# Optimization experiments

Measured on AMD Instinct MI355X. Metric: run time of the kernel, lower is better.

Reference implementation:

```python
import jax, jax.numpy as jnp
import numpy as np

B, P, D, VP, VD = 256, 1152, 10, 8, 16
NUM_ITER = 3


def setup_inputs() -> dict:
    key = jax.random.key(0)
    k1, k2 = jax.random.split(key)
    x = jax.random.normal(k1, (B, P, VP, 1), dtype=jnp.float32)
    # learned transform matrices, init randn/100 as in the torch module
    W = jax.random.normal(k2, (P, D, VD, VP), dtype=jnp.float32) / 100.0
    return {"x": x, "W": W}


def _squash(s, axis):
    # v = ||s||^2/(1+||s||^2) * s/||s||
    sq = jnp.sum(s * s, axis=axis, keepdims=True)
    return s * sq / (1.0 + sq) / jnp.sqrt(sq + 1e-9)


def reference(x, W):
    xs = x[..., 0]                                      # [B,P,8]
    # u_hat[b,p,d,:] = W[p,d] @ x[b,p]  (no explicit stack/broadcast materialization)
    u_hat = jnp.einsum('pdij,bpj->bpdi', W, xs)          # [B,P,D,16]
    u_stop = jax.lax.stop_gradient(u_hat)
    b_ij = jnp.zeros((B, P, D, 1), dtype=u_hat.dtype)    # torch b_ij [B,P,D,1,1], trailing 1 dropped
    v = None
    for it in range(NUM_ITER):
        # faithful to source: softmax over torch dim=3 (size-1 axis) -> all ones
        c_ij = jax.nn.softmax(b_ij, axis=3)               # [B,P,D,1]
        u = u_hat if it == NUM_ITER - 1 else u_stop
        s_j = jnp.sum(c_ij * u, axis=1)                   # [B,D,16]
        v = _squash(s_j, axis=2)                          # [B,D,16]
        if it != NUM_ITER - 1:
            # agreement: u_hat^T v -> scalar per (b,p,d)
            upd = jnp.einsum('bpdi,bdi->bpd', u_hat, v)[..., None]
            b_ij = b_ij + upd
    return v[..., None]                                   # [B,D,16,1] matching torch output
```

## Files before the change

kernel.cpp:

```cpp
#include <hip/hip_runtime.h>
#include <hip/hip_bf16.h>
#include <math.h>

#define M 256
#define N 160
#define K 9216
#define CH 72
#define KC 128
#define BM 32
#define WPS 1296
#define XSTR 136

using f32x4 = __attribute__((ext_vector_type(4))) float;
using bf16x8 = __attribute__((ext_vector_type(8))) short;

__device__ __forceinline__ ushort f2bf(float f) {
  return __builtin_bit_cast(ushort, __float2bfloat16(f));
}

template <bool ATOMIC>
__global__ __launch_bounds__(256) void gemm_mfma(const float* __restrict__ x,
                                                 const float* __restrict__ W,
                                                 float* __restrict__ part) {
  __shared__ __align__(16) ushort Wl[2][4 * WPS];
  __shared__ __align__(16) ushort Xl[BM * XSTR];

  const int t = threadIdx.x;
  const int bx = blockIdx.x;
  const int mt = bx & 7;
  const int c = bx >> 3;
  const int m0 = mt * BM;
  const int k0 = c * KC;

  const int w = t >> 6;
  const int l = t & 63;
  const int lr = l & 15;
  const int lg = l >> 4;
  const int msub = w & 1;
  const int nh = w >> 1;

  {
    const float* xs = x + (size_t)m0 * K + k0;
#pragma unroll
    for (int q = 0; q < 4; ++q) {
      const int f = t + 256 * q;
      const int row = f >> 5;
      const int kq4 = f & 31;
      const float4 v = *(const float4*)(xs + (size_t)row * K + kq4 * 4);
      ushort4 h = {f2bf(v.x), f2bf(v.y), f2bf(v.z), f2bf(v.w)};
      *(ushort4*)&Xl[row * XSTR + kq4 * 4] = h;
    }
  }

  float4 wv[5];
  auto loadW = [&](int s) {
    const float* wsp = W + ((size_t)c * 16 + s * 4) * 1280;
#pragma unroll
    for (int q = 0; q < 5; ++q)
      wv[q] = *(const float4*)(wsp + 4 * (size_t)(t + 256 * q));
  };
  auto putW = [&](int b) {
#pragma unroll
    for (int q = 0; q < 5; ++q) {
      const int e = t + 256 * q;
      const int pl = e / 320;
      const int r4 = e - pl * 320;
      ushort4 h = {f2bf(wv[q].x), f2bf(wv[q].y), f2bf(wv[q].z), f2bf(wv[q].w)};
      *(ushort4*)&Wl[b][pl * WPS + r4 * 4] = h;
    }
  };

  f32x4 acc[5];
#pragma unroll
  for (int nt = 0; nt < 5; ++nt) acc[nt] = {0.f, 0.f, 0.f, 0.f};

  auto comp = [&](int b, int s) {
    const bf16x8 a =
        *(const bf16x8*)&Xl[(msub * 16 + lr) * XSTR + s * 32 + lg * 8];
#pragma unroll
    for (int nt = 0; nt < 5; ++nt) {
      const bf16x8 bb =
          *(const bf16x8*)&Wl[b][lg * WPS + (nh * 5 + nt) * 128 + lr * 8];
      acc[nt] = __builtin_amdgcn_mfma_f32_16x16x32_bf16(a, bb, acc[nt], 0, 0, 0);
    }
  };

  loadW(0);
  putW(0);
  __syncthreads();
  loadW(1);
  comp(0, 0);
  putW(1);
  __syncthreads();
  loadW(2);
  comp(1, 1);
  putW(0);
  __syncthreads();
  loadW(3);
  comp(0, 2);
  putW(1);
  __syncthreads();
  comp(1, 3);

  if (ATOMIC) {
#pragma unroll
    for (int nt = 0; nt < 5; ++nt)
#pragma unroll
      for (int r = 0; r < 4; ++r) {
        const int row = m0 + msub * 16 + lg * 4 + r;
        atomicAdd(&part[(size_t)row * N + (nh * 5 + nt) * 16 + lr],
                  acc[nt][r]);
      }
  } else {
    float* dst = part + (size_t)c * (M * N);
#pragma unroll
    for (int nt = 0; nt < 5; ++nt)
#pragma unroll
      for (int r = 0; r < 4; ++r) {
        const int row = m0 + msub * 16 + lg * 4 + r;
        dst[(size_t)row * N + (nh * 5 + nt) * 16 + lr] = acc[nt][r];
      }
  }
}

__global__ __launch_bounds__(256) void reduce_squash4(
    const float* __restrict__ part, float* __restrict__ out) {
  __shared__ f32x4 red[256];
  const int t = threadIdx.x;
  const int o4 = t & 63;
  const int slice = t >> 6;
  const f32x4* p4 = (const f32x4*)part;
  const int base4 = blockIdx.x * 64;

  f32x4 sum = {0.f, 0.f, 0.f, 0.f};
#pragma unroll 6
  for (int cc = 0; cc < 18; ++cc) {
    const int c = slice * 18 + cc;
    sum += p4[(size_t)c * (M * N / 4) + base4 + o4];
  }
  red[t] = sum;
  __syncthreads();
  if (t < 64) {
    const f32x4 s = red[t] + red[t + 64] + red[t + 128] + red[t + 192];
    float n2 = s[0] * s[0] + s[1] * s[1] + s[2] * s[2] + s[3] * s[3];
    n2 += __shfl_xor(n2, 1);
    n2 += __shfl_xor(n2, 2);
    const float sc = n2 / (1.0f + n2) / sqrtf(n2 + 1e-9f);
    f32x4 o = {s[0] * sc, s[1] * sc, s[2] * sc, s[3] * sc};
    ((f32x4*)out)[base4 + t] = o;
  }
}

__global__ __launch_bounds__(256) void squash_k(float* __restrict__ out) {
  const int e = blockIdx.x * 256 + threadIdx.x;
  const float s = out[e];
  float s2 = s * s;
  s2 += __shfl_xor(s2, 1);
  s2 += __shfl_xor(s2, 2);
  s2 += __shfl_xor(s2, 4);
  s2 += __shfl_xor(s2, 8);
  out[e] = s * s2 / (1.0f + s2) / sqrtf(s2 + 1e-9f);
}

extern "C" void kernel_launch(void* const* d_in, const int* in_sizes, int n_in,
                              void* d_out, int out_size, void* d_ws,
                              size_t ws_size, hipStream_t stream) {
  const float* x = (const float*)d_in[0];
  const float* W = (const float*)d_in[1];
  float* out = (float*)d_out;

  const size_t need = (size_t)CH * M * N * sizeof(float);
  if (ws_size >= need) {
    gemm_mfma<false><<<8 * CH, 256, 0, stream>>>(x, W, (float*)d_ws);
    reduce_squash4<<<(M * N) / 256, 256, 0, stream>>>((const float*)d_ws, out);
  } else {
    hipMemsetAsync(out, 0, (size_t)M * N * sizeof(float), stream);
    gemm_mfma<true><<<8 * CH, 256, 0, stream>>>(x, W, out);
    squash_k<<<(M * N) / 256, 256, 0, stream>>>(out);
  }
}
```

Measured before the change: 20.73 us.

## Double M tile per block and load whole W chunk once

```diff
diff --git a/kernel.cpp b/kernel.cpp
--- a/kernel.cpp
+++ b/kernel.cpp
@@ -7,8 +7,8 @@
 #define K 9216
 #define CH 72
 #define KC 128
-#define BM 32
-#define WPS 1296
+#define BM 64
+#define WPS 1288
 #define XSTR 136
 
 using f32x4 = __attribute__((ext_vector_type(4))) float;
@@ -19,16 +19,16 @@
 }
 
 template <bool ATOMIC>
-__global__ __launch_bounds__(256) void gemm_mfma(const float* __restrict__ x,
+__global__ __launch_bounds__(512) void gemm_mfma(const float* __restrict__ x,
                                                  const float* __restrict__ W,
                                                  float* __restrict__ part) {
-  __shared__ __align__(16) ushort Wl[2][4 * WPS];
+  __shared__ __align__(16) ushort Wl[16 * WPS];
   __shared__ __align__(16) ushort Xl[BM * XSTR];
 
   const int t = threadIdx.x;
   const int bx = blockIdx.x;
-  const int mt = bx & 7;
-  const int c = bx >> 3;
+  const int mt = bx & 3;
+  const int c = bx >> 2;
   const int m0 = mt * BM;
   const int k0 = c * KC;
 
@@ -36,71 +36,60 @@
   const int l = t & 63;
   const int lr = l & 15;
   const int lg = l >> 4;
-  const int msub = w & 1;
-  const int nh = w >> 1;
+  const int msub = w & 3;
+  const int nh = w >> 2;
 
+  float4 wv[10], xv[4];
   {
+    const float* wsp = W + (size_t)c * 16 * 1280;
+#pragma unroll
+    for (int q = 0; q < 10; ++q)
+      wv[q] = *(const float4*)(wsp + 4 * (size_t)(t + 512 * q));
     const float* xs = x + (size_t)m0 * K + k0;
 #pragma unroll
     for (int q = 0; q < 4; ++q) {
-      const int f = t + 256 * q;
+      const int f = t + 512 * q;
       const int row = f >> 5;
-      const int kq4 = f & 31;
-      const float4 v = *(const float4*)(xs + (size_t)row * K + kq4 * 4);
-      ushort4 h = {f2bf(v.x), f2bf(v.y), f2bf(v.z), f2bf(v.w)};
-      *(ushort4*)&Xl[row * XSTR + kq4 * 4] = h;
+      const int k4 = f & 31;
+      xv[q] = *(const float4*)(xs + (size_t)row * K + k4 * 4);
     }
   }
-
-  float4 wv[5];
-  auto loadW = [&](int s) {
-    const float* wsp = W + ((size_t)c * 16 + s * 4) * 1280;
+  {
 #pragma unroll
-    for (int q = 0; q < 5; ++q)
-      wv[q] = *(const float4*)(wsp + 4 * (size_t)(t + 256 * q));
-  };
-  auto putW = [&](int b) {
+    for (int q = 0; q < 10; ++q) {
+      const int f = t + 512 * q;
+      const int pl = f / 320;
+      const int r4 = f - pl * 320;
+      ushort4 h = {f2bf(wv[q].x), f2bf(wv[q].y), f2bf(wv[q].z), f2bf(wv[q].w)};
+      *(ushort4*)&Wl[pl * WPS + r4 * 4] = h;
+    }
 #pragma unroll
-    for (int q = 0; q < 5; ++q) {
-      const int e = t + 256 * q;
-      const int pl = e / 320;
-      const int r4 = e - pl * 320;
-      ushort4 h = {f2bf(wv[q].x), f2bf(wv[q].y), f2bf(wv[q].z), f2bf(wv[q].w)};
-      *(ushort4*)&Wl[b][pl * WPS + r4 * 4] = h;
+    for (int q = 0; q < 4; ++q) {
+      const int f = t + 512 * q;
+      const int row = f >> 5;
+      const int k4 = f & 31;
+      ushort4 h = {f2bf(xv[q].x), f2bf(xv[q].y), f2bf(xv[q].z), f2bf(xv[q].w)};
+      *(ushort4*)&Xl[row * XSTR + k4 * 4] = h;
     }
-  };
+  }
+  __syncthreads();
 
   f32x4 acc[5];
 #pragma unroll
   for (int nt = 0; nt < 5; ++nt) acc[nt] = {0.f, 0.f, 0.f, 0.f};
 
-  auto comp = [&](int b, int s) {
+#pragma unroll
+  for (int ks = 0; ks < 4; ++ks) {
     const bf16x8 a =
-        *(const bf16x8*)&Xl[(msub * 16 + lr) * XSTR + s * 32 + lg * 8];
+        *(const bf16x8*)&Xl[(msub * 16 + lr) * XSTR + ks * 32 + lg * 8];
 #pragma unroll
     for (int nt = 0; nt < 5; ++nt) {
-      const bf16x8 bb =
-          *(const bf16x8*)&Wl[b][lg * WPS + (nh * 5 + nt) * 128 + lr * 8];
-      acc[nt] = __builtin_amdgcn_mfma_f32_16x16x32_bf16(a, bb, acc[nt], 0, 0, 0);
+      const bf16x8 b =
+          *(const bf16x8*)&Wl[(ks * 4 + lg) * WPS + (nh * 5 + nt) * 128 +
+                              lr * 8];
+      acc[nt] = __builtin_amdgcn_mfma_f32_16x16x32_bf16(a, b, acc[nt], 0, 0, 0);
     }
-  };
-
-  loadW(0);
-  putW(0);
-  __syncthreads();
-  loadW(1);
-  comp(0, 0);
-  putW(1);
-  __syncthreads();
-  loadW(2);
-  comp(1, 1);
-  putW(0);
-  __syncthreads();
-  loadW(3);
-  comp(0, 2);
-  putW(1);
-  __syncthreads();
-  comp(1, 3);
+  }
 
   if (ATOMIC) {
 #pragma unroll
@@ -171,11 +160,11 @@
 
   const size_t need = (size_t)CH * M * N * sizeof(float);
   if (ws_size >= need) {
-    gemm_mfma<false><<<8 * CH, 256, 0, stream>>>(x, W, (float*)d_ws);
+    gemm_mfma<false><<<4 * CH, 512, 0, stream>>>(x, W, (float*)d_ws);
     reduce_squash4<<<(M * N) / 256, 256, 0, stream>>>((const float*)d_ws, out);
   } else {
     hipMemsetAsync(out, 0, (size_t)M * N * sizeof(float), stream);
-    gemm_mfma<true><<<8 * CH, 256, 0, stream>>>(x, W, out);
+    gemm_mfma<true><<<4 * CH, 512, 0, stream>>>(x, W, out);
     squash_k<<<(M * N) / 256, 256, 0, stream>>>(out);
   }
 }
```

Result: faster. 18.90 us (-8.8%).
